# Kernel tuning notes

Hardware: AMD Instinct MI355X
Metric: run time of the kernel (lower is better)

## Reference

```python
import jax, jax.numpy as jnp
import numpy as np

B, T, DIM = 4, 1024, 1024
COND = 1024
HEADS, DH = 16, 64
INNER = HEADS * DH
MLP = 4096
EPS = 1e-5


def setup_inputs() -> dict:
    key = jax.random.key(0)
    ks = jax.random.split(key, 12)
    s = 0.02
    return {
        "x": jax.random.normal(ks[0], (B, T, DIM), jnp.float32),
        "c": jax.random.normal(ks[1], (B, 1, COND), jnp.float32),
        # AdaLN modulation Linear (zero-init in the original; randomized here to exercise all paths)
        "W_mod": jax.random.normal(ks[2], (COND, 6 * DIM), jnp.float32) * s,
        "b_mod": jax.random.normal(ks[3], (6 * DIM,), jnp.float32) * s,
        # attention
        "W_qkv": jax.random.normal(ks[4], (DIM, 3 * INNER), jnp.float32) * s,
        "W_out": jax.random.normal(ks[5], (INNER, DIM), jnp.float32) * s,
        "b_out": jax.random.normal(ks[6], (DIM,), jnp.float32) * s,
        # feed-forward
        "W1": jax.random.normal(ks[7], (DIM, MLP), jnp.float32) * s,
        "b1": jax.random.normal(ks[8], (MLP,), jnp.float32) * s,
        "W2": jax.random.normal(ks[9], (MLP, DIM), jnp.float32) * s,
        "b2": jax.random.normal(ks[10], (DIM,), jnp.float32) * s,
    }


def _layernorm(x):
    # affine-free LayerNorm over last dim
    mu = jnp.mean(x, axis=-1, keepdims=True)
    var = jnp.mean(jnp.square(x - mu), axis=-1, keepdims=True)
    return (x - mu) * jax.lax.rsqrt(var + EPS)


def _modulate(x, shift, scale):
    return x * (1.0 + scale) + shift


def _attention(x, W_qkv, W_out, b_out):
    Bq, Tq, _ = x.shape
    qkv = x @ W_qkv  # [B,T,3*INNER]
    q, k, v = jnp.split(qkv, 3, axis=-1)
    q = q.reshape(Bq, Tq, HEADS, DH)
    k = k.reshape(Bq, Tq, HEADS, DH)
    v = v.reshape(Bq, Tq, HEADS, DH)
    scale = DH ** -0.5
    attn = jnp.einsum("bqhd,bkhd->bhqk", q, k) * scale
    attn = jax.nn.softmax(attn, axis=-1)
    out = jnp.einsum("bhqk,bkhd->bqhd", attn, v).reshape(Bq, Tq, INNER)
    return out @ W_out + b_out


def _ff(x, W1, b1, W2, b2):
    return jax.nn.gelu(x @ W1 + b1, approximate=False) @ W2 + b2


def reference(x, c, W_mod, b_mod, W_qkv, W_out, b_out, W1, b1, W2, b2):
    mod = jax.nn.silu(c) @ W_mod + b_mod  # [B,1,6*DIM]
    sh_msa, sc_msa, g_msa, sh_mlp, sc_mlp, g_mlp = jnp.split(mod, 6, axis=-1)
    x = x + g_msa * _attention(_modulate(_layernorm(x), sh_msa, sc_msa), W_qkv, W_out, b_out)
    x = x + g_mlp * _ff(_modulate(_layernorm(x), sh_mlp, sc_mlp), W1, b1, W2, b2)
    return x
```

## Files before the change

kernel.cpp:

```cpp
#include <hip/hip_runtime.h>
#include <hip/hip_bf16.h>
#include <math.h>

#define BB 4
#define TT 1024
#define DIM 1024
#define HEADS 16
#define DH 64
#define INNER 1024
#define MLP 4096

#define OFF_SH_MSA 0
#define OFF_SC_MSA 1024
#define OFF_G_MSA  2048
#define OFF_SH_MLP 3072
#define OFF_SC_MLP 4096
#define OFF_G_MLP  5120

typedef __attribute__((ext_vector_type(8))) short bf16x8;
typedef __attribute__((ext_vector_type(4))) float fx4;

__device__ __forceinline__ unsigned short f2bf(float f) {
    __hip_bfloat16 h = __float2bfloat16(f);
    return __builtin_bit_cast(unsigned short, h);
}
__device__ __forceinline__ float bflo(unsigned u) { return __uint_as_float(u << 16); }
__device__ __forceinline__ float bfhi(unsigned u) { return __uint_as_float(u & 0xffff0000u); }

__device__ __forceinline__ void gload_lds16(const void* g, void* l) {
    __builtin_amdgcn_global_load_lds((const __attribute__((address_space(1))) void*)g,
                                     (__attribute__((address_space(3))) void*)l, 16, 0, 0);
}

__global__ __launch_bounds__(256) void mod_partial(
    const float* __restrict__ c, const float* __restrict__ W_mod,
    float* __restrict__ part)
{
    __shared__ float sc[BB][128];
    int tid = threadIdx.x;
    int ks = blockIdx.y;
    int k0 = ks * 128;
    for (int i = tid; i < BB * 128; i += 256) {
        int bq = i >> 7, kk = i & 127;
        float v = c[bq * 1024 + k0 + kk];
        sc[bq][kk] = v / (1.0f + __expf(-v));
    }
    __syncthreads();
    int n = blockIdx.x * 256 + tid;
    float a0 = 0.f, a1 = 0.f, a2 = 0.f, a3 = 0.f;
    for (int kk = 0; kk < 128; kk++) {
        float w = W_mod[(size_t)(k0 + kk) * 6144 + n];
        a0 += sc[0][kk] * w;
        a1 += sc[1][kk] * w;
        a2 += sc[2][kk] * w;
        a3 += sc[3][kk] * w;
    }
    float* p = part + (size_t)ks * 4 * 6144 + n;
    p[0]        = a0;
    p[6144]     = a1;
    p[2 * 6144] = a2;
    p[3 * 6144] = a3;
}

__global__ __launch_bounds__(256) void mod_reduce(
    const float* __restrict__ part, const float* __restrict__ b_mod,
    float* __restrict__ mod)
{
    int n = blockIdx.x * 256 + threadIdx.x;
    float bb = b_mod[n];
    #pragma unroll
    for (int bq = 0; bq < 4; bq++) {
        float a = bb;
        #pragma unroll
        for (int ks = 0; ks < 8; ks++) a += part[(size_t)(ks * 4 + bq) * 6144 + n];
        mod[bq * 6144 + n] = a;
    }
}

__global__ __launch_bounds__(256) void ln_mod_kernel(
    const float* __restrict__ x, const float* __restrict__ mod,
    int sh_off, int sc_off, unsigned short* __restrict__ out)
{
    int row = blockIdx.x;
    int b = row >> 10;
    const float* xr = x + (size_t)row * DIM;
    float4 v = ((const float4*)xr)[threadIdx.x];

    float s1 = v.x + v.y + v.z + v.w;
    float s2 = v.x * v.x + v.y * v.y + v.z * v.z + v.w * v.w;
    #pragma unroll
    for (int off = 32; off > 0; off >>= 1) {
        s1 += __shfl_down(s1, off, 64);
        s2 += __shfl_down(s2, off, 64);
    }
    __shared__ float red[8];
    int lane = threadIdx.x & 63, w = threadIdx.x >> 6;
    if (lane == 0) { red[w] = s1; red[4 + w] = s2; }
    __syncthreads();
    s1 = red[0] + red[1] + red[2] + red[3];
    s2 = red[4] + red[5] + red[6] + red[7];
    float mu = s1 * (1.0f / DIM);
    float var = s2 * (1.0f / DIM) - mu * mu;
    float rs = rsqrtf(var + 1e-5f);

    int col = threadIdx.x * 4;
    const float* mb = mod + (size_t)b * 6144;
    float4 sc4 = *(const float4*)(mb + sc_off + col);
    float4 sh4 = *(const float4*)(mb + sh_off + col);
    ushort4 o;
    o.x = f2bf((v.x - mu) * rs * (1.0f + sc4.x) + sh4.x);
    o.y = f2bf((v.y - mu) * rs * (1.0f + sc4.y) + sh4.y);
    o.z = f2bf((v.z - mu) * rs * (1.0f + sc4.z) + sh4.z);
    o.w = f2bf((v.w - mu) * rs * (1.0f + sc4.w) + sh4.w);
    ((ushort4*)(out + (size_t)row * DIM))[threadIdx.x] = o;
}

__global__ __launch_bounds__(256) void wcvt_kernel(
    const float* __restrict__ W, unsigned short* __restrict__ Wt, int K, int N)
{
    __shared__ float tile[32][33];
    int n0 = blockIdx.x * 32, k0 = blockIdx.y * 32;
    int tx = threadIdx.x & 31, ty = threadIdx.x >> 5;
    #pragma unroll
    for (int i = 0; i < 4; i++)
        tile[ty + i * 8][tx] = W[(size_t)(k0 + ty + i * 8) * N + n0 + tx];
    __syncthreads();
    #pragma unroll
    for (int i = 0; i < 4; i++)
        Wt[(size_t)(n0 + ty + i * 8) * K + k0 + tx] = f2bf(tile[tx][ty + i * 8]);
}

template<int EPI, int OBF>
__global__ __launch_bounds__(256) void bgemm(
    const unsigned short* __restrict__ A, const unsigned short* __restrict__ Bt,
    const float* __restrict__ bias, const float* __restrict__ res,
    const float* __restrict__ mod, int gate_off,
    void* __restrict__ Cout, int M, int N, int K)
{
    __shared__ unsigned short Atile[128 * 32];
    __shared__ unsigned short Btile[128 * 32];
    const int tid = threadIdx.x;
    const int lane = tid & 63, wid = tid >> 6;
    const int row0 = blockIdx.y * 128, col0 = blockIdx.x * 128;
    const int wr = wid >> 1, wc = wid & 1;

    fx4 acc[4][4];
    const fx4 zero = {0.f, 0.f, 0.f, 0.f};
    #pragma unroll
    for (int m = 0; m < 4; m++)
        #pragma unroll
        for (int n = 0; n < 4; n++) acc[m][n] = zero;

    const int kg = (lane >> 4) * 8;
    const int rl = lane & 15;

    for (int k0 = 0; k0 < K; k0 += 32) {
        #pragma unroll
        for (int i = 0; i < 2; i++) {
            int chunk = wid + i * 4;
            int eo = chunk * 512 + lane * 8;
            int r = eo >> 5, cc = eo & 31;
            gload_lds16(A  + (size_t)(row0 + r) * K + k0 + cc, Atile + eo);
            gload_lds16(Bt + (size_t)(col0 + r) * K + k0 + cc, Btile + eo);
        }
        __syncthreads();

        bf16x8 af[4], bfr[4];
        #pragma unroll
        for (int m = 0; m < 4; m++)
            af[m] = *(const bf16x8*)(Atile + (wr * 64 + m * 16 + rl) * 32 + kg);
        #pragma unroll
        for (int n = 0; n < 4; n++)
            bfr[n] = *(const bf16x8*)(Btile + (wc * 64 + n * 16 + rl) * 32 + kg);
        #pragma unroll
        for (int m = 0; m < 4; m++)
            #pragma unroll
            for (int n = 0; n < 4; n++)
                acc[m][n] = __builtin_amdgcn_mfma_f32_16x16x32_bf16(
                    af[m], bfr[n], acc[m][n], 0, 0, 0);
        __syncthreads();
    }

    const int b = row0 >> 10;
    const int lrow = (lane >> 4) * 4;
    #pragma unroll
    for (int m = 0; m < 4; m++) {
        #pragma unroll
        for (int n = 0; n < 4; n++) {
            int col = col0 + wc * 64 + n * 16 + rl;
            float bv = 0.f, gate = 0.f;
            if (EPI != 0) bv = bias[col];
            if (EPI == 2) gate = mod[(size_t)b * 6144 + gate_off + col];
            #pragma unroll
            for (int j = 0; j < 4; j++) {
                int row = row0 + wr * 64 + m * 16 + lrow + j;
                float v = acc[m][n][j];
                if (EPI == 1) {
                    float u = v + bv;
                    v = 0.5f * u * (1.0f + erff(u * 0.70710678118654752f));
                } else if (EPI == 2) {
                    v = res[(size_t)row * N + col] + gate * (v + bv);
                }
                if (OBF) ((unsigned short*)Cout)[(size_t)row * N + col] = f2bf(v);
                else     ((float*)Cout)[(size_t)row * N + col] = v;
            }
        }
    }
}

__global__ __launch_bounds__(256) void attn_mfma(
    const unsigned short* __restrict__ qkv, unsigned short* __restrict__ out)
{
    __shared__ unsigned short K_l[64 * 64];
    __shared__ unsigned short VT_l[64 * 64];
    __shared__ unsigned short P_l[4 * 16 * 64];

    const int tid = threadIdx.x;
    const int lane = tid & 63, w = tid >> 6;
    const int rl = lane & 15, lg = lane >> 4;
    const int qi = blockIdx.x & 15;
    const int bh = blockIdx.x >> 4;
    const int b = bh >> 4, h = bh & 15;

    const unsigned short* base = qkv + (size_t)b * TT * 3 * INNER + h * DH;

    const int qrow = qi * 64 + w * 16 + rl;
    bf16x8 qf[2];
    qf[0] = *(const bf16x8*)(base + (size_t)qrow * 3 * INNER + lg * 8);
    qf[1] = *(const bf16x8*)(base + (size_t)qrow * 3 * INNER + lg * 8 + 32);

    const fx4 z4 = {0.f, 0.f, 0.f, 0.f};
    fx4 acc_o[4];
    #pragma unroll
    for (int db = 0; db < 4; db++) acc_o[db] = z4;
    float mrow[4] = {-INFINITY, -INFINITY, -INFINITY, -INFINITY};
    float lrow[4] = {0.f, 0.f, 0.f, 0.f};

    unsigned short* Pw = P_l + w * 1024;

    for (int kt = 0; kt < 16; kt++) {
        __syncthreads();
        #pragma unroll
        for (int i = 0; i < 2; i++) {
            int instr = w * 2 + i;
            int row = instr * 8 + (lane >> 3);
            int slog = (lane & 7) ^ (lane >> 3);
            gload_lds16(base + (size_t)(kt * 64 + row) * 3 * INNER + INNER + slog * 8,
                        K_l + instr * 512);
        }
        #pragma unroll
        for (int hh = 0; hh < 2; hh++) {
            int dc = tid & 7;
            int kr = (tid >> 3) + hh * 32;
            const unsigned short* vg =
                base + (size_t)(kt * 64 + kr) * 3 * INNER + 2 * INNER + dc * 8;
            uint4 vv = *(const uint4*)vg;
            unsigned wds[4] = {vv.x, vv.y, vv.z, vv.w};
            #pragma unroll
            for (int j = 0; j < 8; j++) {
                unsigned word = wds[j >> 1];
                unsigned short e = (j & 1) ? (unsigned short)(word >> 16)
                                           : (unsigned short)(word & 0xffff);
                int d = dc * 8 + j;
                int phys = ((kr >> 3) ^ j ^ dc) & 7;
                VT_l[d * 64 + phys * 8 + (kr & 7)] = e;
            }
        }
        __syncthreads();

        fx4 sacc[4];
        #pragma unroll
        for (int kb = 0; kb < 4; kb++) sacc[kb] = z4;
        #pragma unroll
        for (int half = 0; half < 2; half++) {
            #pragma unroll
            for (int kb = 0; kb < 4; kb++) {
                int kr = kb * 16 + rl;
                bf16x8 kf = *(const bf16x8*)(
                    K_l + kr * 64 + (((lg + half * 4) ^ (kr & 7)) & 7) * 8);
                sacc[kb] = __builtin_amdgcn_mfma_f32_16x16x32_bf16(
                    qf[half], kf, sacc[kb], 0, 0, 0);
            }
        }

        #pragma unroll
        for (int kb = 0; kb < 4; kb++) sacc[kb] *= 0.125f;

        float f[4], p[4][4];
        #pragma unroll
        for (int j = 0; j < 4; j++) {
            float t = fmaxf(fmaxf(sacc[0][j], sacc[1][j]),
                            fmaxf(sacc[2][j], sacc[3][j]));
            t = fmaxf(t, __shfl_xor(t, 1));
            t = fmaxf(t, __shfl_xor(t, 2));
            t = fmaxf(t, __shfl_xor(t, 4));
            t = fmaxf(t, __shfl_xor(t, 8));
            float nm = fmaxf(mrow[j], t);
            f[j] = __expf(mrow[j] - nm);
            mrow[j] = nm;
        }
        #pragma unroll
        for (int kb = 0; kb < 4; kb++)
            #pragma unroll
            for (int j = 0; j < 4; j++)
                p[kb][j] = __expf(sacc[kb][j] - mrow[j]);
        #pragma unroll
        for (int j = 0; j < 4; j++) {
            float s = (p[0][j] + p[1][j]) + (p[2][j] + p[3][j]);
            s += __shfl_xor(s, 1);
            s += __shfl_xor(s, 2);
            s += __shfl_xor(s, 4);
            s += __shfl_xor(s, 8);
            lrow[j] = lrow[j] * f[j] + s;
        }
        fx4 fv = {f[0], f[1], f[2], f[3]};
        #pragma unroll
        for (int db = 0; db < 4; db++) acc_o[db] *= fv;

        #pragma unroll
        for (int kb = 0; kb < 4; kb++) {
            #pragma unroll
            for (int j = 0; j < 4; j++) {
                int q16 = lg * 4 + j;
                int phys = ((kb * 2 + (rl >> 3)) ^ (q16 & 7)) & 7;
                Pw[q16 * 64 + phys * 8 + (rl & 7)] = f2bf(p[kb][j]);
            }
        }
        asm volatile("s_waitcnt lgkmcnt(0)" ::: "memory");

        #pragma unroll
        for (int half = 0; half < 2; half++) {
            bf16x8 pf = *(const bf16x8*)(
                Pw + rl * 64 + (((lg + half * 4) ^ (rl & 7)) & 7) * 8);
            #pragma unroll
            for (int db = 0; db < 4; db++) {
                int d = db * 16 + rl;
                bf16x8 vf = *(const bf16x8*)(
                    VT_l + d * 64 +
                    ((((lg + half * 4) ^ (d & 7)) ^ ((d >> 3) & 7)) & 7) * 8);
                acc_o[db] = __builtin_amdgcn_mfma_f32_16x16x32_bf16(
                    pf, vf, acc_o[db], 0, 0, 0);
            }
        }
    }

    float inv[4];
    #pragma unroll
    for (int j = 0; j < 4; j++) inv[j] = 1.0f / lrow[j];
    #pragma unroll
    for (int db = 0; db < 4; db++) {
        #pragma unroll
        for (int j = 0; j < 4; j++) {
            int row = qi * 64 + w * 16 + lg * 4 + j;
            out[(size_t)(b * TT + row) * INNER + h * DH + db * 16 + rl] =
                f2bf(acc_o[db][j] * inv[j]);
        }
    }
}

extern "C" void kernel_launch(void* const* d_in, const int* in_sizes, int n_in,
                              void* d_out, int out_size, void* d_ws, size_t ws_size,
                              hipStream_t stream)
{
    const float* x     = (const float*)d_in[0];
    const float* c     = (const float*)d_in[1];
    const float* W_mod = (const float*)d_in[2];
    const float* b_mod = (const float*)d_in[3];
    const float* W_qkv = (const float*)d_in[4];
    const float* W_out = (const float*)d_in[5];
    const float* b_out = (const float*)d_in[6];
    const float* W1    = (const float*)d_in[7];
    const float* b1    = (const float*)d_in[8];
    const float* W2    = (const float*)d_in[9];
    const float* b2    = (const float*)d_in[10];
    float* out = (float*)d_out;

    const int M = BB * TT;

    char* ws = (char*)d_ws;
    float* mod      = (float*)ws;
    float* mod_part = (float*)(ws + 131072);
    float* x1       = (float*)(ws + 1048576);
    unsigned short* bb = (unsigned short*)(ws + 1048576 + (size_t)M * DIM * 4);
    unsigned short* Wqkv_t = bb;  bb += (size_t)3 * INNER * DIM;
    unsigned short* Wout_t = bb;  bb += (size_t)DIM * INNER;
    unsigned short* W1_t   = bb;  bb += (size_t)MLP * DIM;
    unsigned short* W2_t   = bb;  bb += (size_t)DIM * MLP;
    unsigned short* xm     = bb;  bb += (size_t)M * DIM;
    unsigned short* qkvb   = bb;  bb += (size_t)M * 3 * INNER;
    unsigned short* attnb  = bb;  bb += (size_t)M * INNER;
    unsigned short* xm2    = bb;  bb += (size_t)M * DIM;
    unsigned short* hbuf   = bb;  bb += (size_t)M * MLP;

    wcvt_kernel<<<dim3(3 * INNER / 32, DIM / 32), 256, 0, stream>>>(W_qkv, Wqkv_t, DIM, 3 * INNER);
    wcvt_kernel<<<dim3(DIM / 32, INNER / 32), 256, 0, stream>>>(W_out, Wout_t, INNER, DIM);
    wcvt_kernel<<<dim3(MLP / 32, DIM / 32), 256, 0, stream>>>(W1, W1_t, DIM, MLP);
    wcvt_kernel<<<dim3(DIM / 32, MLP / 32), 256, 0, stream>>>(W2, W2_t, MLP, DIM);

    mod_partial<<<dim3(24, 8), 256, 0, stream>>>(c, W_mod, mod_part);
    mod_reduce<<<24, 256, 0, stream>>>(mod_part, b_mod, mod);
    ln_mod_kernel<<<M, 256, 0, stream>>>(x, mod, OFF_SH_MSA, OFF_SC_MSA, xm);
    bgemm<0, 1><<<dim3(3 * INNER / 128, M / 128), 256, 0, stream>>>(
        xm, Wqkv_t, nullptr, nullptr, nullptr, 0, qkvb, M, 3 * INNER, DIM);
    attn_mfma<<<BB * HEADS * (TT / 64), 256, 0, stream>>>(qkvb, attnb);
    bgemm<2, 0><<<dim3(DIM / 128, M / 128), 256, 0, stream>>>(
        attnb, Wout_t, b_out, x, mod, OFF_G_MSA, x1, M, DIM, INNER);
    ln_mod_kernel<<<M, 256, 0, stream>>>(x1, mod, OFF_SH_MLP, OFF_SC_MLP, xm2);
    bgemm<1, 1><<<dim3(MLP / 128, M / 128), 256, 0, stream>>>(
        xm2, W1_t, b1, nullptr, nullptr, 0, hbuf, M, MLP, DIM);
    bgemm<2, 0><<<dim3(DIM / 128, M / 128), 256, 0, stream>>>(
        hbuf, W2_t, b2, x1, mod, OFF_G_MLP, out, M, DIM, MLP);
}
```

Measured before the change: 465.6 us.

## Merge weight conversions, narrow N-tiles for DIM-output GEMMs, and swizzle workgroup order

The four weight transpose/convert launches become one kernel that dispatches on block index. The GEMM gains an NF template parameter, so the two GEMMs with 1024-wide output use 128x64 tiles and launch twice as many workgroups, improving occupancy across the CUs. A block-index swizzle that interleaves groups of eight is added to the GEMM and attention kernels, intended to spread neighbouring tiles across XCDs and improve L2 locality. Narrower tiles give less reuse per loaded A tile, and the swizzle assumes the workgroup count is divisible by eight.

Measured after the change: 436.9 us. 1.07x faster.

```diff
diff --git a/kernel.cpp b/kernel.cpp
--- a/kernel.cpp
+++ b/kernel.cpp
@@ -24,8 +24,6 @@
     __hip_bfloat16 h = __float2bfloat16(f);
     return __builtin_bit_cast(unsigned short, h);
 }
-__device__ __forceinline__ float bflo(unsigned u) { return __uint_as_float(u << 16); }
-__device__ __forceinline__ float bfhi(unsigned u) { return __uint_as_float(u & 0xffff0000u); }
 
 __device__ __forceinline__ void gload_lds16(const void* g, void* l) {
     __builtin_amdgcn_global_load_lds((const __attribute__((address_space(1))) void*)g,
@@ -115,11 +113,20 @@
     ((ushort4*)(out + (size_t)row * DIM))[threadIdx.x] = o;
 }
 
-__global__ __launch_bounds__(256) void wcvt_kernel(
-    const float* __restrict__ W, unsigned short* __restrict__ Wt, int K, int N)
+__global__ __launch_bounds__(256) void wcvt_all(
+    const float* __restrict__ Wqkv, const float* __restrict__ Wout,
+    const float* __restrict__ W1,   const float* __restrict__ W2,
+    unsigned short* __restrict__ oQ, unsigned short* __restrict__ oO,
+    unsigned short* __restrict__ o1, unsigned short* __restrict__ o2)
 {
     __shared__ float tile[32][33];
-    int n0 = blockIdx.x * 32, k0 = blockIdx.y * 32;
+    int t = blockIdx.x;
+    const float* W; unsigned short* O; int K, N, nx;
+    if (t < 3072)      {            W = Wqkv; O = oQ; K = 1024; N = 3072; nx = 96;  }
+    else if (t < 4096) { t -= 3072; W = Wout; O = oO; K = 1024; N = 1024; nx = 32;  }
+    else if (t < 8192) { t -= 4096; W = W1;   O = o1; K = 1024; N = 4096; nx = 128; }
+    else               { t -= 8192; W = W2;   O = o2; K = 4096; N = 1024; nx = 32;  }
+    int n0 = (t % nx) * 32, k0 = (t / nx) * 32;
     int tx = threadIdx.x & 31, ty = threadIdx.x >> 5;
     #pragma unroll
     for (int i = 0; i < 4; i++)
@@ -127,10 +134,10 @@
     __syncthreads();
     #pragma unroll
     for (int i = 0; i < 4; i++)
-        Wt[(size_t)(n0 + ty + i * 8) * K + k0 + tx] = f2bf(tile[tx][ty + i * 8]);
-}
-
-template<int EPI, int OBF>
+        O[(size_t)(n0 + ty + i * 8) * K + k0 + tx] = f2bf(tile[tx][ty + i * 8]);
+}
+
+template<int EPI, int OBF, int NF>
 __global__ __launch_bounds__(256) void bgemm(
     const unsigned short* __restrict__ A, const unsigned short* __restrict__ Bt,
     const float* __restrict__ bias, const float* __restrict__ res,
@@ -138,18 +145,25 @@
     void* __restrict__ Cout, int M, int N, int K)
 {
     __shared__ unsigned short Atile[128 * 32];
-    __shared__ unsigned short Btile[128 * 32];
+    __shared__ unsigned short Btile[NF * 32 * 32];
     const int tid = threadIdx.x;
     const int lane = tid & 63, wid = tid >> 6;
-    const int row0 = blockIdx.y * 128, col0 = blockIdx.x * 128;
+
+    const int gx = gridDim.x;
+    const int nwg = gx * gridDim.y;
+    const int bid = blockIdx.y * gx + blockIdx.x;
+    const int swz = (bid & 7) * (nwg >> 3) + (bid >> 3);
+    const int row0 = (swz / gx) * 128;
+    const int col0 = (swz % gx) * (NF * 32);
+
     const int wr = wid >> 1, wc = wid & 1;
 
-    fx4 acc[4][4];
+    fx4 acc[4][NF];
     const fx4 zero = {0.f, 0.f, 0.f, 0.f};
     #pragma unroll
     for (int m = 0; m < 4; m++)
         #pragma unroll
-        for (int n = 0; n < 4; n++) acc[m][n] = zero;
+        for (int n = 0; n < NF; n++) acc[m][n] = zero;
 
     const int kg = (lane >> 4) * 8;
     const int rl = lane & 15;
@@ -160,22 +174,28 @@
             int chunk = wid + i * 4;
             int eo = chunk * 512 + lane * 8;
             int r = eo >> 5, cc = eo & 31;
-            gload_lds16(A  + (size_t)(row0 + r) * K + k0 + cc, Atile + eo);
+            gload_lds16(A + (size_t)(row0 + r) * K + k0 + cc, Atile + eo);
+        }
+        #pragma unroll
+        for (int i = 0; i < (NF >> 1); i++) {
+            int chunk = wid + i * 4;
+            int eo = chunk * 512 + lane * 8;
+            int r = eo >> 5, cc = eo & 31;
             gload_lds16(Bt + (size_t)(col0 + r) * K + k0 + cc, Btile + eo);
         }
         __syncthreads();
 
-        bf16x8 af[4], bfr[4];
+        bf16x8 af[4], bfr[NF];
         #pragma unroll
         for (int m = 0; m < 4; m++)
             af[m] = *(const bf16x8*)(Atile + (wr * 64 + m * 16 + rl) * 32 + kg);
         #pragma unroll
-        for (int n = 0; n < 4; n++)
-            bfr[n] = *(const bf16x8*)(Btile + (wc * 64 + n * 16 + rl) * 32 + kg);
+        for (int n = 0; n < NF; n++)
+            bfr[n] = *(const bf16x8*)(Btile + (wc * (NF * 16) + n * 16 + rl) * 32 + kg);
         #pragma unroll
         for (int m = 0; m < 4; m++)
             #pragma unroll
-            for (int n = 0; n < 4; n++)
+            for (int n = 0; n < NF; n++)
                 acc[m][n] = __builtin_amdgcn_mfma_f32_16x16x32_bf16(
                     af[m], bfr[n], acc[m][n], 0, 0, 0);
         __syncthreads();
@@ -186,8 +206,8 @@
     #pragma unroll
     for (int m = 0; m < 4; m++) {
         #pragma unroll
-        for (int n = 0; n < 4; n++) {
-            int col = col0 + wc * 64 + n * 16 + rl;
+        for (int n = 0; n < NF; n++) {
+            int col = col0 + wc * (NF * 16) + n * 16 + rl;
             float bv = 0.f, gate = 0.f;
             if (EPI != 0) bv = bias[col];
             if (EPI == 2) gate = mod[(size_t)b * 6144 + gate_off + col];
@@ -218,8 +238,11 @@
     const int tid = threadIdx.x;
     const int lane = tid & 63, w = tid >> 6;
     const int rl = lane & 15, lg = lane >> 4;
-    const int qi = blockIdx.x & 15;
-    const int bh = blockIdx.x >> 4;
+
+    const int bid = blockIdx.x;
+    const int swz = (bid & 7) * 128 + (bid >> 3);
+    const int qi = swz & 15;
+    const int bh = swz >> 4;
     const int b = bh >> 4, h = bh & 15;
 
     const unsigned short* base = qkv + (size_t)b * TT * 3 * INNER + h * DH;
@@ -392,22 +415,20 @@
     unsigned short* xm2    = bb;  bb += (size_t)M * DIM;
     unsigned short* hbuf   = bb;  bb += (size_t)M * MLP;
 
-    wcvt_kernel<<<dim3(3 * INNER / 32, DIM / 32), 256, 0, stream>>>(W_qkv, Wqkv_t, DIM, 3 * INNER);
-    wcvt_kernel<<<dim3(DIM / 32, INNER / 32), 256, 0, stream>>>(W_out, Wout_t, INNER, DIM);
-    wcvt_kernel<<<dim3(MLP / 32, DIM / 32), 256, 0, stream>>>(W1, W1_t, DIM, MLP);
-    wcvt_kernel<<<dim3(DIM / 32, MLP / 32), 256, 0, stream>>>(W2, W2_t, MLP, DIM);
+    wcvt_all<<<12288, 256, 0, stream>>>(W_qkv, W_out, W1, W2,
+                                        Wqkv_t, Wout_t, W1_t, W2_t);
 
     mod_partial<<<dim3(24, 8), 256, 0, stream>>>(c, W_mod, mod_part);
     mod_reduce<<<24, 256, 0, stream>>>(mod_part, b_mod, mod);
     ln_mod_kernel<<<M, 256, 0, stream>>>(x, mod, OFF_SH_MSA, OFF_SC_MSA, xm);
-    bgemm<0, 1><<<dim3(3 * INNER / 128, M / 128), 256, 0, stream>>>(
+    bgemm<0, 1, 4><<<dim3(3 * INNER / 128, M / 128), 256, 0, stream>>>(
         xm, Wqkv_t, nullptr, nullptr, nullptr, 0, qkvb, M, 3 * INNER, DIM);
     attn_mfma<<<BB * HEADS * (TT / 64), 256, 0, stream>>>(qkvb, attnb);
-    bgemm<2, 0><<<dim3(DIM / 128, M / 128), 256, 0, stream>>>(
+    bgemm<2, 0, 2><<<dim3(DIM / 64, M / 128), 256, 0, stream>>>(
         attnb, Wout_t, b_out, x, mod, OFF_G_MSA, x1, M, DIM, INNER);
     ln_mod_kernel<<<M, 256, 0, stream>>>(x1, mod, OFF_SH_MLP, OFF_SC_MLP, xm2);
-    bgemm<1, 1><<<dim3(MLP / 128, M / 128), 256, 0, stream>>>(
+    bgemm<1, 1, 4><<<dim3(MLP / 128, M / 128), 256, 0, stream>>>(
         xm2, W1_t, b1, nullptr, nullptr, 0, hbuf, M, MLP, DIM);
-    bgemm<2, 0><<<dim3(DIM / 128, M / 128), 256, 0, stream>>>(
+    bgemm<2, 0, 2><<<dim3(DIM / 64, M / 128), 256, 0, stream>>>(
         hbuf, W2_t, b2, x1, mod, OFF_G_MLP, out, M, DIM, MLP);
 }
```
